# Kernel optimization log

Hardware: AMD Instinct MI355X
Metric: run time of the kernel (lower is better)

Reference implementation:

```python
import jax, jax.numpy as jnp
import numpy as np

G, P, D, K, H = 256, 1024, 128, 16, 32  # graphs, nodes/graph, feat dim, clusters, MLP hidden
N = G * P


def setup_inputs() -> dict:
    key = jax.random.key(0)
    k0, k1, k2 = jax.random.split(key, 3)
    node_feats = jax.random.normal(k0, (N, D), dtype=jnp.float32)
    W1 = jax.random.normal(k1, (D, H), dtype=jnp.float32) * (1.0 / np.sqrt(D))
    b1 = jnp.zeros((H,), dtype=jnp.float32)
    W2 = jax.random.normal(k2, (H, K), dtype=jnp.float32) * (1.0 / np.sqrt(H))
    b2 = jnp.zeros((K,), dtype=jnp.float32)
    n_node = jnp.full((G,), P, dtype=jnp.int32)
    return {"node_feats": node_feats, "W1": W1, "b1": b1, "W2": W2, "b2": b2, "n_node": n_node}


def reference(node_feats, W1, b1, W2, b2, n_node):
    num_nodes = node_feats.shape[0]
    num_graphs = n_node.shape[0]
    num_clusters = W2.shape[1]

    # MLP([32, K]) assignment logits + softmax
    h = jax.nn.relu(node_feats @ W1 + b1)
    assignments = jax.nn.softmax(h @ W2 + b2, axis=-1)  # [N, K]

    # graph id per node
    batch_indices = jnp.repeat(jnp.arange(num_graphs), n_node, total_repeat_length=num_nodes)

    # per-cluster weighted segment_sum (loop over small fixed K, as in the original)
    coarse = [
        jax.ops.segment_sum(node_feats * assignments[:, k:k + 1], batch_indices, num_segments=num_graphs)
        for k in range(num_clusters)
    ]
    coarse_nodes = jnp.stack(coarse, axis=1).reshape(-1, node_feats.shape[-1])  # [G*K, D]

    # fully-connected coarse edges per graph (nonzero of ones is row-major: sender repeated, receiver tiled)
    single_senders = jnp.repeat(jnp.arange(num_clusters), num_clusters)
    single_receivers = jnp.tile(jnp.arange(num_clusters), num_clusters)
    batch_offset = jnp.arange(num_graphs)[:, None] * num_clusters
    c_senders = (single_senders[None, :] + batch_offset).reshape(-1)
    c_receivers = (single_receivers[None, :] + batch_offset).reshape(-1)
    c_edges = jnp.ones((c_senders.shape[0], 1), dtype=node_feats.dtype)

    return coarse_nodes, assignments, c_senders, c_receivers, c_edges
```

## Files before the change

### kernel.cpp

```cpp
#include <hip/hip_runtime.h>
#include <hip/hip_bf16.h>
#include <cstdint>

#define G_ 256
#define P_ 1024
#define D_ 128
#define K_ 16
#define H_ 32
#define N_ (G_ * P_)

constexpr size_t OFF_COARSE = 0;
constexpr size_t OFF_ASSIGN = (size_t)G_ * K_ * D_;
constexpr size_t OFF_SEND   = OFF_ASSIGN + (size_t)N_ * K_;
constexpr size_t OFF_RECV   = OFF_SEND + (size_t)G_ * K_ * K_;
constexpr size_t OFF_EDGE   = OFF_RECV + (size_t)G_ * K_ * K_;

typedef __attribute__((ext_vector_type(8))) short bf16x8;
typedef __attribute__((ext_vector_type(4))) float f32x4;

__device__ __forceinline__ void splitf(float x, short& h, short& l) {
    const unsigned u = __float_as_uint(x);
    h = (short)(u >> 16);
    const float hf = __uint_as_float(u & 0xffff0000u);
    const float r = x - hf;
    l = (short)(__float_as_uint(r) >> 16);
}

__global__ __launch_bounds__(256, 2) void mlp_assign_mfma(
    const float* __restrict__ x, const float* __restrict__ W1,
    const float* __restrict__ b1, const float* __restrict__ W2,
    const float* __restrict__ b2, float* __restrict__ assign_out)
{
    __shared__ float hlds[4][64 * 36];

    const int tid  = threadIdx.x;
    const int lane = tid & 63;
    const int wave = tid >> 6;
    const int q = lane >> 4;
    const int c = lane & 15;

    bf16x8 w1h[4][2], w1l[4][2];
#pragma unroll
    for (int kb = 0; kb < 4; ++kb)
#pragma unroll
        for (int nt = 0; nt < 2; ++nt)
#pragma unroll
            for (int e = 0; e < 8; ++e) {
                const int k = kb * 32 + q * 8 + e;
                short hb, lb; splitf(W1[k * H_ + nt * 16 + c], hb, lb);
                w1h[kb][nt][e] = hb; w1l[kb][nt][e] = lb;
            }
    bf16x8 w2h, w2l;
#pragma unroll
    for (int e = 0; e < 8; ++e) {
        short hb, lb; splitf(W2[(q * 8 + e) * K_ + c], hb, lb);
        w2h[e] = hb; w2l[e] = lb;
    }
    const float b1v0 = b1[c];
    const float b1v1 = b1[16 + c];
    const float b2v  = b2[c];

    const size_t base = (size_t)blockIdx.x * 256 + (size_t)wave * 64;

    f32x4 acc[4][2];
#pragma unroll
    for (int mt = 0; mt < 4; ++mt) {
        acc[mt][0] = f32x4{b1v0, b1v0, b1v0, b1v0};
        acc[mt][1] = f32x4{b1v1, b1v1, b1v1, b1v1};
    }
#pragma unroll
    for (int kb = 0; kb < 4; ++kb) {
        bf16x8 ah[4], al[4];
#pragma unroll
        for (int mt = 0; mt < 4; ++mt) {
            const float* rp = x + (base + mt * 16 + c) * D_ + kb * 32 + q * 8;
            const float4 v0 = *(const float4*)rp;
            const float4 v1 = *(const float4*)(rp + 4);
            const float vv[8] = {v0.x, v0.y, v0.z, v0.w, v1.x, v1.y, v1.z, v1.w};
#pragma unroll
            for (int e = 0; e < 8; ++e) {
                short hb, lb; splitf(vv[e], hb, lb);
                ah[mt][e] = hb; al[mt][e] = lb;
            }
        }
#pragma unroll
        for (int mt = 0; mt < 4; ++mt)
#pragma unroll
            for (int nt = 0; nt < 2; ++nt) {
                acc[mt][nt] = __builtin_amdgcn_mfma_f32_16x16x32_bf16(ah[mt], w1h[kb][nt], acc[mt][nt], 0, 0, 0);
                acc[mt][nt] = __builtin_amdgcn_mfma_f32_16x16x32_bf16(ah[mt], w1l[kb][nt], acc[mt][nt], 0, 0, 0);
                acc[mt][nt] = __builtin_amdgcn_mfma_f32_16x16x32_bf16(al[mt], w1h[kb][nt], acc[mt][nt], 0, 0, 0);
            }
    }

    float* hl = &hlds[wave][0];
#pragma unroll
    for (int mt = 0; mt < 4; ++mt)
#pragma unroll
        for (int nt = 0; nt < 2; ++nt)
#pragma unroll
            for (int r = 0; r < 4; ++r)
                hl[(mt * 16 + q * 4 + r) * 36 + nt * 16 + c] = fmaxf(acc[mt][nt][r], 0.f);

    f32x4 lacc[4];
#pragma unroll
    for (int mt = 0; mt < 4; ++mt) lacc[mt] = f32x4{b2v, b2v, b2v, b2v};
#pragma unroll
    for (int mt = 0; mt < 4; ++mt) {
        const float* rp = hl + (mt * 16 + c) * 36 + q * 8;
        const float4 v0 = *(const float4*)rp;
        const float4 v1 = *(const float4*)(rp + 4);
        const float vv[8] = {v0.x, v0.y, v0.z, v0.w, v1.x, v1.y, v1.z, v1.w};
        bf16x8 ah, al;
#pragma unroll
        for (int e = 0; e < 8; ++e) {
            short hb, lb; splitf(vv[e], hb, lb);
            ah[e] = hb; al[e] = lb;
        }
        lacc[mt] = __builtin_amdgcn_mfma_f32_16x16x32_bf16(ah, w2h, lacc[mt], 0, 0, 0);
        lacc[mt] = __builtin_amdgcn_mfma_f32_16x16x32_bf16(ah, w2l, lacc[mt], 0, 0, 0);
        lacc[mt] = __builtin_amdgcn_mfma_f32_16x16x32_bf16(al, w2h, lacc[mt], 0, 0, 0);
    }

#pragma unroll
    for (int mt = 0; mt < 4; ++mt)
#pragma unroll
        for (int r = 0; r < 4; ++r) {
            const float v = lacc[mt][r];
            float mx = v;
#pragma unroll
            for (int s = 1; s < 16; s <<= 1) mx = fmaxf(mx, __shfl_xor(mx, s, 16));
            const float e = __expf(v - mx);
            float sum = e;
#pragma unroll
            for (int s = 1; s < 16; s <<= 1) sum += __shfl_xor(sum, s, 16);
            assign_out[(base + mt * 16 + q * 4 + r) * K_ + c] = e / sum;
        }
}

#define FMA4(dst, v, sc)                                                      \
    dst.x = fmaf(v.x, sc, dst.x); dst.y = fmaf(v.y, sc, dst.y);               \
    dst.z = fmaf(v.z, sc, dst.z); dst.w = fmaf(v.w, sc, dst.w)

__global__ __launch_bounds__(1024, 4) void coarse_kernel(
    const float* __restrict__ x, const float* __restrict__ assign,
    const int* __restrict__ n_node, float* __restrict__ coarse)
{
    __shared__ float xs[2][32 * 128];
    __shared__ float as_[2][32 * 16];
    __shared__ int pref[G_];

    const int tid = threadIdx.x;

    if (tid < G_) pref[tid] = n_node[tid];
    __syncthreads();
    for (int st = 1; st < G_; st <<= 1) {
        int v = 0;
        if (tid < G_ && tid >= st) v = pref[tid - st];
        __syncthreads();
        if (tid < G_ && tid >= st) pref[tid] += v;
        __syncthreads();
    }
    const int g = blockIdx.x;
    const int start = (g == 0) ? 0 : min(pref[g - 1], N_);
    const int end   = (g == G_ - 1) ? N_ : min(pref[g], N_);

    const int dq = tid & 31;
    const int s  = tid >> 5;

    float4 acc[K_];
#pragma unroll
    for (int k = 0; k < K_; ++k) acc[k] = make_float4(0.f, 0.f, 0.f, 0.f);

    const int total = end - start;
    const int nfull = total >> 5;
    const int tail  = total & 31;

    float4 rx = make_float4(0.f, 0.f, 0.f, 0.f);
    float4 ra = make_float4(0.f, 0.f, 0.f, 0.f);
    if (nfull > 0) {
        rx = *(const float4*)(x + (size_t)start * D_ + tid * 4);
        if (tid < 128)
            ra = *(const float4*)(assign + (size_t)start * K_ + tid * 4);
    }

    int b = 0;
    for (int c = 0; c < nfull; ++c) {
        *(float4*)(&xs[b][tid * 4]) = rx;
        if (tid < 128) *(float4*)(&as_[b][tid * 4]) = ra;
        __syncthreads();

        if (c + 1 < nfull) {
            const size_t nb = (size_t)start + (size_t)(c + 1) * 32;
            rx = *(const float4*)(x + nb * D_ + tid * 4);
            if (tid < 128)
                ra = *(const float4*)(assign + nb * K_ + tid * 4);
        }

        const float4 xv = *(const float4*)(&xs[b][s * D_ + dq * 4]);
        const float4* av = (const float4*)(&as_[b][s * K_]);
#pragma unroll
        for (int qq = 0; qq < 4; ++qq) {
            const float4 a = av[qq];
            FMA4(acc[4 * qq + 0], xv, a.x);
            FMA4(acc[4 * qq + 1], xv, a.y);
            FMA4(acc[4 * qq + 2], xv, a.z);
            FMA4(acc[4 * qq + 3], xv, a.w);
        }
        b ^= 1;
    }

    if (tail > 0 && s < tail) {
        const size_t n = (size_t)start + (size_t)nfull * 32 + s;
        const float4 xv = *(const float4*)(x + n * D_ + dq * 4);
        const float4* av = (const float4*)(assign + n * K_);
#pragma unroll
        for (int qq = 0; qq < 4; ++qq) {
            const float4 a = av[qq];
            FMA4(acc[4 * qq + 0], xv, a.x);
            FMA4(acc[4 * qq + 1], xv, a.y);
            FMA4(acc[4 * qq + 2], xv, a.z);
            FMA4(acc[4 * qq + 3], xv, a.w);
        }
    }

    __syncthreads();
    float* red = &xs[0][0];
#pragma unroll
    for (int k = 0; k < K_; ++k) {
        *(float4*)(&red[s * D_ + dq * 4]) = acc[k];
        __syncthreads();
        if (tid < D_) {
            float sum = 0.f;
#pragma unroll
            for (int ss = 0; ss < 32; ++ss) sum += red[ss * D_ + tid];
            coarse[((size_t)g * K_ + k) * D_ + tid] = sum;
        }
        __syncthreads();
    }
}

__global__ __launch_bounds__(256) void edges_kernel(float* __restrict__ out)
{
    const int e = blockIdx.x * 256 + threadIdx.x;
    const int g = e >> 8;
    const int pair = e & 255;
    const int i = pair >> 4;
    const int j = pair & 15;
    out[OFF_SEND + e] = (float)(g * K_ + i);
    out[OFF_RECV + e] = (float)(g * K_ + j);
    out[OFF_EDGE + e] = 1.0f;
}

extern "C" void kernel_launch(void* const* d_in, const int* in_sizes, int n_in,
                              void* d_out, int out_size, void* d_ws, size_t ws_size,
                              hipStream_t stream)
{
    const float* x      = (const float*)d_in[0];
    const float* W1     = (const float*)d_in[1];
    const float* b1     = (const float*)d_in[2];
    const float* W2     = (const float*)d_in[3];
    const float* b2     = (const float*)d_in[4];
    const int*   n_node = (const int*)d_in[5];
    float* out = (float*)d_out;

    mlp_assign_mfma<<<N_ / 256, 256, 0, stream>>>(x, W1, b1, W2, b2, out + OFF_ASSIGN);
    coarse_kernel<<<G_, 1024, 0, stream>>>(x, out + OFF_ASSIGN, n_node, out + OFF_COARSE);
    edges_kernel<<<(G_ * K_ * K_) / 256, 256, 0, stream>>>(out);
}
```

Measured before the change: 64.34 us.

## Stage MLP input via swizzled LDS with coalesced prefetch and fold edges into coarse kernel

The MLP kernel now loads each 16-row tile of node features with fully coalesced float4 loads, stages it through XOR-swizzled shared memory, and prefetches the next tile while computing the current one. The hidden activations are stored already split into bf16 hi/lo pairs. Processing one tile at a time lowers register pressure, so the occupancy hint is raised from 2 to 3 blocks. The separate edges kernel is removed and its writes move into the coarse kernel, saving one launch; the cost is extra LDS traffic and more synchronisation-sensitive code.

Result: slower. 78.83 us (+22.5%).

```diff
diff --git a/kernel.cpp b/kernel.cpp
--- a/kernel.cpp
+++ b/kernel.cpp
@@ -26,12 +26,13 @@
     l = (short)(__float_as_uint(r) >> 16);
 }
 
-__global__ __launch_bounds__(256, 2) void mlp_assign_mfma(
+__global__ __launch_bounds__(256, 3) void mlp_assign_mfma(
     const float* __restrict__ x, const float* __restrict__ W1,
     const float* __restrict__ b1, const float* __restrict__ W2,
     const float* __restrict__ b2, float* __restrict__ assign_out)
 {
-    __shared__ float hlds[4][64 * 36];
+    __shared__ float    xstage[4][2048];
+    __shared__ unsigned hstage[4][512];
 
     const int tid  = threadIdx.x;
     const int lane = tid & 63;
@@ -46,87 +47,107 @@
         for (int nt = 0; nt < 2; ++nt)
 #pragma unroll
             for (int e = 0; e < 8; ++e) {
-                const int k = kb * 32 + q * 8 + e;
-                short hb, lb; splitf(W1[k * H_ + nt * 16 + c], hb, lb);
+                short hb, lb;
+                splitf(W1[(kb * 32 + q * 8 + e) * H_ + nt * 16 + c], hb, lb);
                 w1h[kb][nt][e] = hb; w1l[kb][nt][e] = lb;
             }
     bf16x8 w2h, w2l;
 #pragma unroll
     for (int e = 0; e < 8; ++e) {
-        short hb, lb; splitf(W2[(q * 8 + e) * K_ + c], hb, lb);
+        short hb, lb;
+        splitf(W2[(q * 8 + e) * K_ + c], hb, lb);
         w2h[e] = hb; w2l[e] = lb;
     }
     const float b1v0 = b1[c];
     const float b1v1 = b1[16 + c];
     const float b2v  = b2[c];
 
-    const size_t base = (size_t)blockIdx.x * 256 + (size_t)wave * 64;
-
-    f32x4 acc[4][2];
+    float* xw = xstage[wave];
+    unsigned* hw = hstage[wave];
+    const size_t nodebase = (size_t)blockIdx.x * 256 + (size_t)wave * 64;
+
+    float4 ld[8];
+    {
+        const float4* src = (const float4*)(x + nodebase * D_);
+#pragma unroll
+        for (int i = 0; i < 8; ++i) ld[i] = src[i * 64 + lane];
+    }
+
 #pragma unroll
     for (int mt = 0; mt < 4; ++mt) {
-        acc[mt][0] = f32x4{b1v0, b1v0, b1v0, b1v0};
-        acc[mt][1] = f32x4{b1v1, b1v1, b1v1, b1v1};
-    }
-#pragma unroll
-    for (int kb = 0; kb < 4; ++kb) {
-        bf16x8 ah[4], al[4];
-#pragma unroll
-        for (int mt = 0; mt < 4; ++mt) {
-            const float* rp = x + (base + mt * 16 + c) * D_ + kb * 32 + q * 8;
-            const float4 v0 = *(const float4*)rp;
-            const float4 v1 = *(const float4*)(rp + 4);
+#pragma unroll
+        for (int i = 0; i < 8; ++i) {
+            const int cid  = i * 64 + lane;
+            const int row  = cid >> 5;
+            const int colf = (cid & 31) * 4;
+            const int kb   = colf >> 5;
+            const int win  = colf & 31;
+            const int addr = (kb * 2048 + row * 128 + win * 4) ^ ((row & 7) << 4);
+            *(float4*)((char*)xw + addr) = ld[i];
+        }
+
+        if (mt < 3) {
+            const float4* src = (const float4*)(x + (nodebase + (size_t)(mt + 1) * 16) * D_);
+#pragma unroll
+            for (int i = 0; i < 8; ++i) ld[i] = src[i * 64 + lane];
+        }
+
+        f32x4 acc0 = {b1v0, b1v0, b1v0, b1v0};
+        f32x4 acc1 = {b1v1, b1v1, b1v1, b1v1};
+#pragma unroll
+        for (int kb = 0; kb < 4; ++kb) {
+            const int rb = kb * 2048 + c * 128 + q * 32;
+            const int sw = (c & 7) << 4;
+            const float4 v0 = *(const float4*)((char*)xw + (rb ^ sw));
+            const float4 v1 = *(const float4*)((char*)xw + ((rb + 16) ^ sw));
             const float vv[8] = {v0.x, v0.y, v0.z, v0.w, v1.x, v1.y, v1.z, v1.w};
+            bf16x8 ah, al;
 #pragma unroll
             for (int e = 0; e < 8; ++e) {
                 short hb, lb; splitf(vv[e], hb, lb);
-                ah[mt][e] = hb; al[mt][e] = lb;
+                ah[e] = hb; al[e] = lb;
             }
-        }
-#pragma unroll
-        for (int mt = 0; mt < 4; ++mt)
-#pragma unroll
-            for (int nt = 0; nt < 2; ++nt) {
-                acc[mt][nt] = __builtin_amdgcn_mfma_f32_16x16x32_bf16(ah[mt], w1h[kb][nt], acc[mt][nt], 0, 0, 0);
-                acc[mt][nt] = __builtin_amdgcn_mfma_f32_16x16x32_bf16(ah[mt], w1l[kb][nt], acc[mt][nt], 0, 0, 0);
-                acc[mt][nt] = __builtin_amdgcn_mfma_f32_16x16x32_bf16(al[mt], w1h[kb][nt], acc[mt][nt], 0, 0, 0);
-            }
-    }
-
-    float* hl = &hlds[wave][0];
-#pragma unroll
-    for (int mt = 0; mt < 4; ++mt)
-#pragma unroll
-        for (int nt = 0; nt < 2; ++nt)
-#pragma unroll
-            for (int r = 0; r < 4; ++r)
-                hl[(mt * 16 + q * 4 + r) * 36 + nt * 16 + c] = fmaxf(acc[mt][nt][r], 0.f);
-
-    f32x4 lacc[4];
-#pragma unroll
-    for (int mt = 0; mt < 4; ++mt) lacc[mt] = f32x4{b2v, b2v, b2v, b2v};
-#pragma unroll
-    for (int mt = 0; mt < 4; ++mt) {
-        const float* rp = hl + (mt * 16 + c) * 36 + q * 8;
-        const float4 v0 = *(const float4*)rp;
-        const float4 v1 = *(const float4*)(rp + 4);
-        const float vv[8] = {v0.x, v0.y, v0.z, v0.w, v1.x, v1.y, v1.z, v1.w};
-        bf16x8 ah, al;
+            acc0 = __builtin_amdgcn_mfma_f32_16x16x32_bf16(ah, w1h[kb][0], acc0, 0, 0, 0);
+            acc0 = __builtin_amdgcn_mfma_f32_16x16x32_bf16(ah, w1l[kb][0], acc0, 0, 0, 0);
+            acc0 = __builtin_amdgcn_mfma_f32_16x16x32_bf16(al, w1h[kb][0], acc0, 0, 0, 0);
+            acc1 = __builtin_amdgcn_mfma_f32_16x16x32_bf16(ah, w1h[kb][1], acc1, 0, 0, 0);
+            acc1 = __builtin_amdgcn_mfma_f32_16x16x32_bf16(ah, w1l[kb][1], acc1, 0, 0, 0);
+            acc1 = __builtin_amdgcn_mfma_f32_16x16x32_bf16(al, w1h[kb][1], acc1, 0, 0, 0);
+        }
+
+#pragma unroll
+        for (int r = 0; r < 4; ++r) {
+            const int row = q * 4 + r;
+            const int xsw = (row & 7) << 2;
+            short hb, lb;
+            const float t0 = fmaxf(acc0[r], 0.f);
+            splitf(t0, hb, lb);
+            hw[(row * 32 + c) ^ xsw] =
+                ((unsigned)(unsigned short)hb << 16) | (unsigned short)lb;
+            const float t1 = fmaxf(acc1[r], 0.f);
+            splitf(t1, hb, lb);
+            hw[(row * 32 + 16 + c) ^ xsw] =
+                ((unsigned)(unsigned short)hb << 16) | (unsigned short)lb;
+        }
+
+        const int hsw = (c & 7) << 2;
+        const uint4 u0 = *(const uint4*)&hw[(c * 32 + q * 8) ^ hsw];
+        const uint4 u1 = *(const uint4*)&hw[(c * 32 + q * 8 + 4) ^ hsw];
+        const unsigned uu[8] = {u0.x, u0.y, u0.z, u0.w, u1.x, u1.y, u1.z, u1.w};
+        bf16x8 ha, la;
 #pragma unroll
         for (int e = 0; e < 8; ++e) {
-            short hb, lb; splitf(vv[e], hb, lb);
-            ah[e] = hb; al[e] = lb;
-        }
-        lacc[mt] = __builtin_amdgcn_mfma_f32_16x16x32_bf16(ah, w2h, lacc[mt], 0, 0, 0);
-        lacc[mt] = __builtin_amdgcn_mfma_f32_16x16x32_bf16(ah, w2l, lacc[mt], 0, 0, 0);
-        lacc[mt] = __builtin_amdgcn_mfma_f32_16x16x32_bf16(al, w2h, lacc[mt], 0, 0, 0);
-    }
-
-#pragma unroll
-    for (int mt = 0; mt < 4; ++mt)
+            ha[e] = (short)(uu[e] >> 16);
+            la[e] = (short)(uu[e] & 0xffffu);
+        }
+        f32x4 lacc = {b2v, b2v, b2v, b2v};
+        lacc = __builtin_amdgcn_mfma_f32_16x16x32_bf16(ha, w2h, lacc, 0, 0, 0);
+        lacc = __builtin_amdgcn_mfma_f32_16x16x32_bf16(ha, w2l, lacc, 0, 0, 0);
+        lacc = __builtin_amdgcn_mfma_f32_16x16x32_bf16(la, w2h, lacc, 0, 0, 0);
+
 #pragma unroll
         for (int r = 0; r < 4; ++r) {
-            const float v = lacc[mt][r];
+            const float v = lacc[r];
             float mx = v;
 #pragma unroll
             for (int s = 1; s < 16; s <<= 1) mx = fmaxf(mx, __shfl_xor(mx, s, 16));
@@ -134,8 +155,9 @@
             float sum = e;
 #pragma unroll
             for (int s = 1; s < 16; s <<= 1) sum += __shfl_xor(sum, s, 16);
-            assign_out[(base + mt * 16 + q * 4 + r) * K_ + c] = e / sum;
-        }
+            assign_out[(nodebase + (size_t)mt * 16 + q * 4 + r) * K_ + c] = e / sum;
+        }
+    }
 }
 
 #define FMA4(dst, v, sc)                                                      \
@@ -144,13 +166,21 @@
 
 __global__ __launch_bounds__(1024, 4) void coarse_kernel(
     const float* __restrict__ x, const float* __restrict__ assign,
-    const int* __restrict__ n_node, float* __restrict__ coarse)
+    const int* __restrict__ n_node, float* __restrict__ out)
 {
     __shared__ float xs[2][32 * 128];
     __shared__ float as_[2][32 * 16];
     __shared__ int pref[G_];
 
     const int tid = threadIdx.x;
+    const int g = blockIdx.x;
+
+    if (tid < 256) {
+        const int e = g * 256 + tid;
+        out[OFF_SEND + e] = (float)(g * K_ + (tid >> 4));
+        out[OFF_RECV + e] = (float)(g * K_ + (tid & 15));
+        out[OFF_EDGE + e] = 1.0f;
+    }
 
     if (tid < G_) pref[tid] = n_node[tid];
     __syncthreads();
@@ -161,7 +191,6 @@
         if (tid < G_ && tid >= st) pref[tid] += v;
         __syncthreads();
     }
-    const int g = blockIdx.x;
     const int start = (g == 0) ? 0 : min(pref[g - 1], N_);
     const int end   = (g == G_ - 1) ? N_ : min(pref[g], N_);
 
@@ -185,13 +214,13 @@
     }
 
     int b = 0;
-    for (int c = 0; c < nfull; ++c) {
+    for (int cc = 0; cc < nfull; ++cc) {
         *(float4*)(&xs[b][tid * 4]) = rx;
         if (tid < 128) *(float4*)(&as_[b][tid * 4]) = ra;
         __syncthreads();
 
-        if (c + 1 < nfull) {
-            const size_t nb = (size_t)start + (size_t)(c + 1) * 32;
+        if (cc + 1 < nfull) {
+            const size_t nb = (size_t)start + (size_t)(cc + 1) * 32;
             rx = *(const float4*)(x + nb * D_ + tid * 4);
             if (tid < 128)
                 ra = *(const float4*)(assign + nb * K_ + tid * 4);
@@ -234,22 +263,10 @@
             float sum = 0.f;
 #pragma unroll
             for (int ss = 0; ss < 32; ++ss) sum += red[ss * D_ + tid];
-            coarse[((size_t)g * K_ + k) * D_ + tid] = sum;
-        }
-        __syncthreads();
-    }
-}
-
-__global__ __launch_bounds__(256) void edges_kernel(float* __restrict__ out)
-{
-    const int e = blockIdx.x * 256 + threadIdx.x;
-    const int g = e >> 8;
-    const int pair = e & 255;
-    const int i = pair >> 4;
-    const int j = pair & 15;
-    out[OFF_SEND + e] = (float)(g * K_ + i);
-    out[OFF_RECV + e] = (float)(g * K_ + j);
-    out[OFF_EDGE + e] = 1.0f;
+            out[OFF_COARSE + ((size_t)g * K_ + k) * D_ + tid] = sum;
+        }
+        __syncthreads();
+    }
 }
 
 extern "C" void kernel_launch(void* const* d_in, const int* in_sizes, int n_in,
@@ -265,6 +282,5 @@
     float* out = (float*)d_out;
 
     mlp_assign_mfma<<<N_ / 256, 256, 0, stream>>>(x, W1, b1, W2, b2, out + OFF_ASSIGN);
-    coarse_kernel<<<G_, 1024, 0, stream>>>(x, out + OFF_ASSIGN, n_node, out + OFF_COARSE);
-    edges_kernel<<<(G_ * K_ * K_) / 256, 256, 0, stream>>>(out);
-}
+    coarse_kernel<<<G_, 1024, 0, stream>>>(x, out + OFF_ASSIGN, n_node, out);
+}
```
